# Optimization experiments

Measured on AMD Instinct MI355X. Metric: run time of the kernel, lower is better.

## Reference

```python
import jax, jax.numpy as jnp
import numpy as np


def _jacobian_circulant(v):
    """Spatial Jacobian of a 3D vector field with circulant boundaries.

    v : (B, X, Y, Z, D) velocity field (channels last)
    returns J : (B, X, Y, Z, D, D) with J[..., i, j] = d v_i / d x_j,
    computed by central differences with wrap-around (circulant) bounds.
    """
    cols = []
    for j in range(3):
        ax = 1 + j  # spatial axis for coordinate j
        g = (jnp.roll(v, -1, axis=ax) - jnp.roll(v, 1, axis=ax)) * 0.5
        cols.append(g)
    return jnp.stack(cols, axis=-1)  # (B, X, Y, Z, D, D)


def _bracket(x, y):
    """Lie bracket of two velocity fields: [x, y] = J_x y - J_y x."""
    jx = _jacobian_circulant(x)
    jy = _jacobian_circulant(y)
    return (jnp.einsum('bxyzij,bxyzj->bxyzi', jx, y)
            - jnp.einsum('bxyzij,bxyzj->bxyzi', jy, x))


def _bch(x, y, trunc=2):
    """Truncated BCH series: z s.t. exp(z) = exp(x) o exp(y)."""
    z = x + y
    if trunc >= 2:
        z = z + 0.5 * _bracket(x, y)
    return z


def setup_inputs() -> dict:
    key = jax.random.key(0)
    k1, k2 = jax.random.split(key)
    B, D, X, Y, Z = 2, 3, 128, 128, 128
    left = jax.random.normal(k1, (B, D, X, Y, Z), dtype=jnp.float32)
    right = jax.random.normal(k2, (B, D, X, Y, Z), dtype=jnp.float32)
    return {"left": left, "right": right}


def reference(left, right):
    # (B, D, *shape) -> channels-last (B, *shape, D)
    l = jnp.moveaxis(left, 1, -1)
    r = jnp.moveaxis(right, 1, -1)
    v = _bch(l, r, trunc=2)
    return jnp.moveaxis(v, -1, 1)
```

## Files before the change

### kernel.cpp

```cpp
#include <hip/hip_runtime.h>


namespace {
constexpr int Xd = 128, Yd = 128, Zd = 128, Bd = 2, Dd = 3;
constexpr int Sd  = Xd * Yd * Zd;
constexpr int YZd = Yd * Zd;

__device__ inline float4 f4sub(float4 a, float4 b) {
    return make_float4(a.x - b.x, a.y - b.y, a.z - b.z, a.w - b.w);
}
__device__ inline float4 f4add(float4 a, float4 b) {
    return make_float4(a.x + b.x, a.y + b.y, a.z + b.z, a.w + b.w);
}
__device__ inline float4 f4mul(float4 a, float4 b) {
    return make_float4(a.x * b.x, a.y * b.y, a.z * b.z, a.w * b.w);
}
__device__ inline float4 f4fma(float4 a, float4 b, float4 c) {
    return make_float4(fmaf(a.x, b.x, c.x), fmaf(a.y, b.y, c.y),
                       fmaf(a.z, b.z, c.z), fmaf(a.w, b.w, c.w));
}
__device__ inline float4 f4fms(float4 a, float4 b, float4 c) {
    return make_float4(fmaf(-a.x, b.x, c.x), fmaf(-a.y, b.y, c.y),
                       fmaf(-a.z, b.z, c.z), fmaf(-a.w, b.w, c.w));
}
}

__global__ void __launch_bounds__(256)
bch_kernel(const float* __restrict__ L, const float* __restrict__ R,
           float* __restrict__ O)
{
    const int tid = blockIdx.x * 256 + threadIdx.x;
    const int z0  = (tid & 31) << 2;
    int t = tid >> 5;
    const int y = t & 127; t >>= 7;
    const int x = t & 127;
    const int b = t >> 7;

    const int base = b * (Dd * Sd) + x * YZd + y * Zd + z0;

    const int oxp = (((x + 1) & 127) - x) * YZd;
    const int oxm = (((x - 1) & 127) - x) * YZd;
    const int oyp = (((y + 1) & 127) - y) * Zd;
    const int oym = (((y - 1) & 127) - y) * Zd;
    const int ozm = ((z0 - 1) & 127) - z0;
    const int ozp = ((z0 + 4) & 127) - z0;

    float4 Lc[3], Rc[3];
#pragma unroll
    for (int d = 0; d < 3; ++d) {
        Lc[d] = *(const float4*)(L + base + d * Sd);
        Rc[d] = *(const float4*)(R + base + d * Sd);
    }

#pragma unroll
    for (int i = 0; i < 3; ++i) {
        const float* lp = L + base + i * Sd;
        const float* rp = R + base + i * Sd;

        float4 dl = f4sub(*(const float4*)(lp + oxp), *(const float4*)(lp + oxm));
        float4 dr = f4sub(*(const float4*)(rp + oxp), *(const float4*)(rp + oxm));
        float4 br = f4fms(dr, Lc[0], f4mul(dl, Rc[0]));

        dl = f4sub(*(const float4*)(lp + oyp), *(const float4*)(lp + oym));
        dr = f4sub(*(const float4*)(rp + oyp), *(const float4*)(rp + oym));
        br = f4fms(dr, Lc[1], f4fma(dl, Rc[1], br));

        const float lzm = lp[ozm], lzp = lp[ozp];
        const float rzm = rp[ozm], rzp = rp[ozp];
        dl = make_float4(Lc[i].y - lzm, Lc[i].z - Lc[i].x,
                         Lc[i].w - Lc[i].y, lzp - Lc[i].z);
        dr = make_float4(Rc[i].y - rzm, Rc[i].z - Rc[i].x,
                         Rc[i].w - Rc[i].y, rzp - Rc[i].z);
        br = f4fms(dr, Lc[2], f4fma(dl, Rc[2], br));

        float4 out = f4add(Lc[i], Rc[i]);
        const float4 q = make_float4(0.25f, 0.25f, 0.25f, 0.25f);
        out = f4fma(q, br, out);

        *(float4*)(O + base + i * Sd) = out;
    }
}

extern "C" void kernel_launch(void* const* d_in, const int* in_sizes, int n_in,
                              void* d_out, int out_size, void* d_ws, size_t ws_size,
                              hipStream_t stream)
{
    const float* L = (const float*)d_in[0];
    const float* R = (const float*)d_in[1];
    float*       O = (float*)d_out;

    const int nthreads = Bd * Xd * Yd * (Zd / 4);
    dim3 grid(nthreads / 256), block(256);
    bch_kernel<<<grid, block, 0, stream>>>(L, R, O);
}
```

Measured before the change: 153.4 us.

## March along x with register rolling window and shared-memory y halo

Replaces the one-thread-per-point stencil with blocks that march over 8 x-planes. Each thread keeps a four-plane register window for the x neighbours. The y neighbours are shared through LDS with halo loads only on the edge rows, and the z neighbours come from wavefront shuffles. This cuts redundant global and L2 loads of neighbouring values, at the cost of higher register pressure, two barriers per plane, and a much smaller grid (512 blocks).

```diff
diff --git a/kernel.cpp b/kernel.cpp
--- a/kernel.cpp
+++ b/kernel.cpp
@@ -2,9 +2,12 @@
 
 
 namespace {
-constexpr int Xd = 128, Yd = 128, Zd = 128, Bd = 2, Dd = 3;
+constexpr int Xd = 128, Yd = 128, Zd = 128, Dd = 3;
 constexpr int Sd  = Xd * Yd * Zd;
 constexpr int YZd = Yd * Zd;
+constexpr int XSEG = 8;
+constexpr int YT   = 8;
+constexpr int ZC   = 32;
 
 __device__ inline float4 f4sub(float4 a, float4 b) {
     return make_float4(a.x - b.x, a.y - b.y, a.z - b.z, a.w - b.w);
@@ -25,59 +28,125 @@
 }
 }
 
-__global__ void __launch_bounds__(256)
-bch_kernel(const float* __restrict__ L, const float* __restrict__ R,
-           float* __restrict__ O)
+__global__ void __launch_bounds__(256, 2)
+bch_march(const float* __restrict__ L, const float* __restrict__ R,
+          float* __restrict__ O)
 {
-    const int tid = blockIdx.x * 256 + threadIdx.x;
-    const int z0  = (tid & 31) << 2;
-    int t = tid >> 5;
-    const int y = t & 127; t >>= 7;
-    const int x = t & 127;
-    const int b = t >> 7;
+    __shared__ float4 sP[2 * Dd][YT][ZC];
 
-    const int base = b * (Dd * Sd) + x * YZd + y * Zd + z0;
+    const int t  = threadIdx.x;
+    const int zc = t & 31;
+    const int ly = t >> 5;
 
-    const int oxp = (((x + 1) & 127) - x) * YZd;
-    const int oxm = (((x - 1) & 127) - x) * YZd;
+    int bb = blockIdx.x;
+    const int xs = bb & 15; bb >>= 4;
+    const int yt = bb & 15; bb >>= 4;
+    const int b  = bb;
+
+    const int y  = yt * YT + ly;
+    const int z0 = zc * 4;
+    const int x0 = xs * XSEG;
+
+    const int fbase = b * (Dd * Sd) + y * Zd + z0;
+    const float* pL = L + fbase;
+    const float* pR = R + fbase;
+    float*       pO = O + fbase;
+
+    const int oym = (((y - 1) & 127) - y) * Zd;
     const int oyp = (((y + 1) & 127) - y) * Zd;
-    const int oym = (((y - 1) & 127) - y) * Zd;
-    const int ozm = ((z0 - 1) & 127) - z0;
-    const int ozp = ((z0 + 4) & 127) - z0;
+    const int zlm = (zc + 31) & 31;
+    const int zlp = (zc + 1) & 31;
 
-    float4 Lc[3], Rc[3];
+    float4 AL[3], AR[3], BL[3], BR[3], CL[3], CR[3], DL[3], DR[3];
+
+    auto loadP = [&](float4 (&PL)[3], float4 (&PR)[3], int xp) {
+        const int off = xp * YZd;
 #pragma unroll
-    for (int d = 0; d < 3; ++d) {
-        Lc[d] = *(const float4*)(L + base + d * Sd);
-        Rc[d] = *(const float4*)(R + base + d * Sd);
-    }
+        for (int d = 0; d < 3; ++d) {
+            PL[d] = *(const float4*)(pL + off + d * Sd);
+            PR[d] = *(const float4*)(pR + off + d * Sd);
+        }
+    };
+
+    loadP(AL, AR, (x0 + 127) & 127);
+    loadP(BL, BR, x0);
+    loadP(CL, CR, (x0 + 1) & 127);
 
 #pragma unroll
-    for (int i = 0; i < 3; ++i) {
-        const float* lp = L + base + i * Sd;
-        const float* rp = R + base + i * Sd;
+    for (int s = 0; s < XSEG; ++s) {
+        const int x    = x0 + s;
+        const int xoff = x * YZd;
 
-        float4 dl = f4sub(*(const float4*)(lp + oxp), *(const float4*)(lp + oxm));
-        float4 dr = f4sub(*(const float4*)(rp + oxp), *(const float4*)(rp + oxm));
-        float4 br = f4fms(dr, Lc[0], f4mul(dl, Rc[0]));
+        if (s < XSEG - 1) loadP(DL, DR, (x + 2) & 127);
 
-        dl = f4sub(*(const float4*)(lp + oyp), *(const float4*)(lp + oym));
-        dr = f4sub(*(const float4*)(rp + oyp), *(const float4*)(rp + oym));
-        br = f4fms(dr, Lc[1], f4fma(dl, Rc[1], br));
+        float4 HmL[3], HmR[3], HpL[3], HpR[3];
+        if (ly == 0) {
+#pragma unroll
+            for (int d = 0; d < 3; ++d) {
+                HmL[d] = *(const float4*)(pL + xoff + oym + d * Sd);
+                HmR[d] = *(const float4*)(pR + xoff + oym + d * Sd);
+            }
+        }
+        if (ly == YT - 1) {
+#pragma unroll
+            for (int d = 0; d < 3; ++d) {
+                HpL[d] = *(const float4*)(pL + xoff + oyp + d * Sd);
+                HpR[d] = *(const float4*)(pR + xoff + oyp + d * Sd);
+            }
+        }
 
-        const float lzm = lp[ozm], lzp = lp[ozp];
-        const float rzm = rp[ozm], rzp = rp[ozp];
-        dl = make_float4(Lc[i].y - lzm, Lc[i].z - Lc[i].x,
-                         Lc[i].w - Lc[i].y, lzp - Lc[i].z);
-        dr = make_float4(Rc[i].y - rzm, Rc[i].z - Rc[i].x,
-                         Rc[i].w - Rc[i].y, rzp - Rc[i].z);
-        br = f4fms(dr, Lc[2], f4fma(dl, Rc[2], br));
+#pragma unroll
+        for (int d = 0; d < 3; ++d) {
+            sP[d][ly][zc]     = BL[d];
+            sP[3 + d][ly][zc] = BR[d];
+        }
+        __syncthreads();
 
-        float4 out = f4add(Lc[i], Rc[i]);
-        const float4 q = make_float4(0.25f, 0.25f, 0.25f, 0.25f);
-        out = f4fma(q, br, out);
+        const int lym = (ly == 0) ? 0 : ly - 1;
+        const int lyp = (ly == YT - 1) ? YT - 1 : ly + 1;
+        float4 yLm[3], yRm[3], yLp[3], yRp[3];
+#pragma unroll
+        for (int d = 0; d < 3; ++d) {
+            yLm[d] = sP[d][lym][zc];     if (ly == 0)      yLm[d] = HmL[d];
+            yRm[d] = sP[3 + d][lym][zc]; if (ly == 0)      yRm[d] = HmR[d];
+            yLp[d] = sP[d][lyp][zc];     if (ly == YT - 1) yLp[d] = HpL[d];
+            yRp[d] = sP[3 + d][lyp][zc]; if (ly == YT - 1) yRp[d] = HpR[d];
+        }
 
-        *(float4*)(O + base + i * Sd) = out;
+#pragma unroll
+        for (int i = 0; i < 3; ++i) {
+            float4 dl = f4sub(CL[i], AL[i]);
+            float4 dr = f4sub(CR[i], AR[i]);
+            float4 br = f4fms(dr, BL[0], f4mul(dl, BR[0]));
+
+            dl = f4sub(yLp[i], yLm[i]);
+            dr = f4sub(yRp[i], yRm[i]);
+            br = f4fms(dr, BL[1], f4fma(dl, BR[1], br));
+
+            const float lzm = __shfl(BL[i].w, zlm, 32);
+            const float lzp = __shfl(BL[i].x, zlp, 32);
+            const float rzm = __shfl(BR[i].w, zlm, 32);
+            const float rzp = __shfl(BR[i].x, zlp, 32);
+            dl = make_float4(BL[i].y - lzm, BL[i].z - BL[i].x,
+                             BL[i].w - BL[i].y, lzp - BL[i].z);
+            dr = make_float4(BR[i].y - rzm, BR[i].z - BR[i].x,
+                             BR[i].w - BR[i].y, rzp - BR[i].z);
+            br = f4fms(dr, BL[2], f4fma(dl, BR[2], br));
+
+            float4 out = f4add(BL[i], BR[i]);
+            const float4 q = make_float4(0.25f, 0.25f, 0.25f, 0.25f);
+            out = f4fma(q, br, out);
+            *(float4*)(pO + xoff + i * Sd) = out;
+        }
+        __syncthreads();
+
+        if (s < XSEG - 1) {
+#pragma unroll
+            for (int d = 0; d < 3; ++d) {
+                AL[d] = BL[d]; BL[d] = CL[d]; CL[d] = DL[d];
+                AR[d] = BR[d]; BR[d] = CR[d]; CR[d] = DR[d];
+            }
+        }
     }
 }
 
@@ -89,7 +158,6 @@
     const float* R = (const float*)d_in[1];
     float*       O = (float*)d_out;
 
-    const int nthreads = Bd * Xd * Yd * (Zd / 4);
-    dim3 grid(nthreads / 256), block(256);
-    bch_kernel<<<grid, block, 0, stream>>>(L, R, O);
+    const int nblocks = 2 * (Yd / YT) * (Xd / XSEG);
+    bch_march<<<dim3(nblocks), dim3(256), 0, stream>>>(L, R, O);
 }
```

After: 141.7 us. 7.6% less time.
